# Kernel tuning notes

Measured on AMD Instinct MI355X. Metric: run time of the kernel, lower is better.

Reference implementation:

```python
import jax, jax.numpy as jnp
import numpy as np

MIN_SIZE = 25.0      # remove_small_boxes threshold (init default)
IOU_THRESH = 0.3     # nms iou_threshold (init default)
MAX_DET = 100        # rcnn_detections_per_image (init default)
IMG = 1024.0         # synthetic image size for box generation


def setup_inputs() -> dict:
    key = jax.random.key(0)
    k1, k2, k3 = jax.random.split(key, 3)
    B, N = 16, 4096
    # valid xyxy boxes inside a 1024x1024 image
    cxcy = jax.random.uniform(k1, (B, N, 2), minval=0.0, maxval=IMG)
    wh = jax.random.uniform(k2, (B, N, 2), minval=1.0, maxval=300.0)
    boxes = jnp.concatenate([cxcy - wh / 2, cxcy + wh / 2], axis=-1)
    boxes = jnp.clip(boxes, 0.0, IMG)
    scores = jax.random.uniform(k3, (B, N))
    return {"boxes": boxes, "scores": scores}


def _pairwise_iou(b):
    # b: [N,4] xyxy -> iou: [N,N]
    area = (b[:, 2] - b[:, 0]) * (b[:, 3] - b[:, 1])
    lt = jnp.maximum(b[:, None, :2], b[None, :, :2])
    rb = jnp.minimum(b[:, None, 2:], b[None, :, 2:])
    wh = jnp.clip(rb - lt, 0.0)
    inter = wh[..., 0] * wh[..., 1]
    return inter / (area[:, None] + area[None, :] - inter + 1e-9)


def _per_image(boxes, scores):
    # boxes [N,4], scores [N] -> (out_boxes [K,4], valid [K])
    N = boxes.shape[0]
    # remove_small_boxes: width and height >= min_size
    valid = ((boxes[:, 2] - boxes[:, 0]) >= MIN_SIZE) & ((boxes[:, 3] - boxes[:, 1]) >= MIN_SIZE)
    s = jnp.where(valid, scores, -jnp.inf)
    order = jnp.argsort(-s)          # score-descending, invalid boxes last
    b = boxes[order]
    v = valid[order]
    iou = _pairwise_iou(b)           # [N,N] dominant intermediate
    idx = jnp.arange(N)

    def body(i, keep):
        # greedy NMS: box i (if kept) suppresses lower-scored overlapping boxes
        sup = (iou[i] > IOU_THRESH) & keep[i] & (idx > i)
        return keep & ~sup

    keep = jax.lax.fori_loop(0, N, body, v)
    # first MAX_DET kept boxes in score order (fixed-shape top-k truncation)
    sel = jnp.argsort(jnp.where(keep, idx, N))[:MAX_DET]
    valid_out = jnp.take(keep, sel)
    out_boxes = jnp.where(valid_out[:, None], b[sel], 0.0)
    return out_boxes, valid_out


def reference(boxes, scores):
    # boxes [B,N,4], scores [B,N] -> [B,K,5] rows (image_idx, x1,y1,x2,y2);
    # padded rows have image_idx = -1 (fixed-shape analogue of the ragged concat)
    out_boxes, valid = jax.vmap(_per_image)(boxes, scores)
    B = boxes.shape[0]
    img_idx = jnp.where(valid, jnp.arange(B, dtype=boxes.dtype)[:, None], -1.0)
    return jnp.concatenate([img_idx[..., None], out_boxes], axis=-1)
```

## Files before the change

### kernel.cpp

```cpp
#include <hip/hip_runtime.h>
#include <math.h>

#define N_BOX 4096
#define B_IMG 16
#define MAXDET 100
#define MINSZ 25.0f
#define IOUT 0.3f
#define IG 16
#define JG 8
#define JW (N_BOX / JG)

__device__ __forceinline__ float iou_f(float ax1, float ay1, float ax2, float ay2, float aarea,
                                       float bx1, float by1, float bx2, float by2, float barea) {
#pragma clang fp contract(off)
    float lx = fmaxf(ax1, bx1);
    float ly = fmaxf(ay1, by1);
    float rx = fminf(ax2, bx2);
    float ry = fminf(ay2, by2);
    float wx = fmaxf(rx - lx, 0.0f);
    float wy = fmaxf(ry - ly, 0.0f);
    float inter = wx * wy;
    float denom = ((aarea + barea) - inter) + 1e-9f;
    return inter / denom;
}

__global__ __launch_bounds__(256) void key_kernel(
        const float4* __restrict__ boxes, const float* __restrict__ scores,
        unsigned long long* __restrict__ ckey) {
    int idx = blockIdx.x * 256 + threadIdx.x;
    float4 bx = boxes[idx];
    bool valid = ((bx.z - bx.x) >= MINSZ) && ((bx.w - bx.y) >= MINSZ);
    float k = valid ? scores[idx] : -INFINITY;
    unsigned u = __float_as_uint(k);
    u = (u & 0x80000000u) ? ~u : (u | 0x80000000u);
    int i = idx & (N_BOX - 1);
    ckey[idx] = ((unsigned long long)u << 12) | (unsigned long long)(N_BOX - 1 - i);
}

__global__ __launch_bounds__(256) void partial_rank_kernel(
        const unsigned long long* __restrict__ ckey, unsigned short* __restrict__ part) {
    int blk = blockIdx.x;
    int jg = blk & (JG - 1);
    int ig = (blk >> 3) & (IG - 1);
    int b  = blk >> 7;
    int t = threadIdx.x;
    int i = ig * 256 + t;
    unsigned long long ci = ckey[b * N_BOX + i];
    const unsigned long long* cj = ckey + b * N_BOX + jg * JW;
    int r = 0;
#pragma unroll 8
    for (int j = 0; j < JW; ++j)
        r += (cj[j] > ci) ? 1 : 0;
    part[(b * JG + jg) * N_BOX + i] = (unsigned short)r;
}

__global__ __launch_bounds__(256) void nms_kernel(
        const float4* __restrict__ boxes, const unsigned long long* __restrict__ ckey,
        const unsigned short* __restrict__ part, float* __restrict__ out) {
    __shared__ unsigned short sinv[N_BOX];
    __shared__ __align__(16) float4 kbox[384];
    __shared__ int scnt[4];
    int b = blockIdx.x;
    int t = threadIdx.x;
    int w = t >> 6, l = t & 63;
    const float4* bb = boxes + (size_t)b * N_BOX;

#pragma unroll
    for (int p = 0; p < 16; ++p) {
        int i = t + 256 * p;
        int rank = 0;
#pragma unroll
        for (int jg = 0; jg < JG; ++jg)
            rank += part[(b * JG + jg) * N_BOX + i];
        unsigned valid = (unsigned)(ckey[b * N_BOX + i] >> 43) & 1u;
        sinv[rank] = (unsigned short)(i | (valid << 15));
    }
    __syncthreads();

    int kept = 0;
    for (int g = 0; g < 16; ++g) {
        int c = g * 4 + w;
        unsigned short e = sinv[c * 64 + l];
        float4 bx = bb[e & 0xFFFu];
        float x1 = bx.x, y1 = bx.y, x2 = bx.z, y2 = bx.w;
        float ar;
        {
#pragma clang fp contract(off)
            ar = (x2 - x1) * (y2 - y1);
        }
        bool alive = (e >> 15) != 0;
        int K0 = kept;
        for (int q = 0; q < K0; ++q) {
            float4 kb = kbox[q];
            float kar;
            {
#pragma clang fp contract(off)
                kar = (kb.z - kb.x) * (kb.w - kb.y);
            }
            float v = iou_f(kb.x, kb.y, kb.z, kb.w, kar, x1, y1, x2, y2, ar);
            if (v > IOUT) alive = false;
        }
        for (int s = 0; s < 4; ++s) {
            if (w == s) {
                int Kcur = K0;
                for (int ss = 0; ss < s; ++ss) Kcur += scnt[ss];
                int cnt = 0;
                if (Kcur < MAXDET) {
                    for (int q = K0; q < Kcur; ++q) {
                        float4 kb = kbox[q];
                        float kar;
                        {
#pragma clang fp contract(off)
                            kar = (kb.z - kb.x) * (kb.w - kb.y);
                        }
                        float v = iou_f(kb.x, kb.y, kb.z, kb.w, kar, x1, y1, x2, y2, ar);
                        if (v > IOUT) alive = false;
                    }
                    unsigned long long m = __ballot(alive);
                    unsigned long long mm = m;
                    while (mm) {
                        int i = __ffsll(mm) - 1;
                        float bx1 = __shfl(x1, i), by1 = __shfl(y1, i);
                        float bx2 = __shfl(x2, i), by2 = __shfl(y2, i);
                        float ba  = __shfl(ar, i);
                        float v = iou_f(bx1, by1, bx2, by2, ba, x1, y1, x2, y2, ar);
                        bool sup = (l > i) && (v > IOUT) && ((m >> l) & 1ull);
                        unsigned long long sm = __ballot(sup);
                        m &= ~sm;
                        mm &= ~(1ull << i);
                        mm &= m;
                    }
                    cnt = __popcll(m);
                    int pos = Kcur + __popcll(m & ((1ull << l) - 1ull));
                    if ((m >> l) & 1ull) kbox[pos] = make_float4(x1, y1, x2, y2);
                }
                if (l == 0) scnt[s] = cnt;
            }
            __syncthreads();
        }
        kept = K0 + scnt[0] + scnt[1] + scnt[2] + scnt[3];
        __syncthreads();
        if (kept >= MAXDET) break;
    }

    int tot = kept < MAXDET ? kept : MAXDET;
    float* ob = out + (size_t)b * MAXDET * 5;
    for (int r = t; r < MAXDET; r += 256) {
        float* row = ob + r * 5;
        if (r < tot) {
            float4 kb = kbox[r];
            row[0] = (float)b;
            row[1] = kb.x; row[2] = kb.y; row[3] = kb.z; row[4] = kb.w;
        } else {
            row[0] = -1.0f;
            row[1] = 0.0f; row[2] = 0.0f; row[3] = 0.0f; row[4] = 0.0f;
        }
    }
}

extern "C" void kernel_launch(void* const* d_in, const int* in_sizes, int n_in,
                              void* d_out, int out_size, void* d_ws, size_t ws_size,
                              hipStream_t stream) {
    const float4* boxes = (const float4*)d_in[0];
    const float* scores = (const float*)d_in[1];
    float* out = (float*)d_out;

    unsigned long long* ckey = (unsigned long long*)d_ws;
    unsigned short* part     = (unsigned short*)((char*)d_ws + (size_t)524288);

    key_kernel<<<B_IMG * N_BOX / 256, 256, 0, stream>>>(boxes, scores, ckey);
    partial_rank_kernel<<<B_IMG * IG * JG, 256, 0, stream>>>(ckey, part);
    nms_kernel<<<B_IMG, 256, 0, stream>>>(boxes, ckey, part, out);
}
```

Before: 114.1 us.

## Fuse key, rank and NMS into one kernel using in-LDS bucket sort

Replaces the three-kernel pipeline (key, O(N^2) pairwise rank, NMS) with one per-image kernel. It builds sort keys in registers, bucket-sorts valid boxes by score into LDS via histogram, prefix scan and atomic scatter, then ranks each box only within its bucket. Invalid boxes are placed after all valid ones by ballot prefix counts. This removes the quadratic rank pass, the global workspace traffic and two launches. In exchange the sort runs on only 16 blocks, and the bucketing assumes scores lie in [0,1).

```diff
diff --git a/kernel.cpp b/kernel.cpp
--- a/kernel.cpp
+++ b/kernel.cpp
@@ -6,9 +6,7 @@
 #define MAXDET 100
 #define MINSZ 25.0f
 #define IOUT 0.3f
-#define IG 16
-#define JG 8
-#define JW (N_BOX / JG)
+#define NBUCK 1024
 
 __device__ __forceinline__ float iou_f(float ax1, float ay1, float ax2, float ay2, float aarea,
                                        float bx1, float by1, float bx2, float by2, float barea) {
@@ -24,56 +22,124 @@
     return inter / denom;
 }
 
-__global__ __launch_bounds__(256) void key_kernel(
+__global__ __launch_bounds__(256) void fused_kernel(
         const float4* __restrict__ boxes, const float* __restrict__ scores,
-        unsigned long long* __restrict__ ckey) {
-    int idx = blockIdx.x * 256 + threadIdx.x;
-    float4 bx = boxes[idx];
-    bool valid = ((bx.z - bx.x) >= MINSZ) && ((bx.w - bx.y) >= MINSZ);
-    float k = valid ? scores[idx] : -INFINITY;
-    unsigned u = __float_as_uint(k);
-    u = (u & 0x80000000u) ? ~u : (u | 0x80000000u);
-    int i = idx & (N_BOX - 1);
-    ckey[idx] = ((unsigned long long)u << 12) | (unsigned long long)(N_BOX - 1 - i);
-}
-
-__global__ __launch_bounds__(256) void partial_rank_kernel(
-        const unsigned long long* __restrict__ ckey, unsigned short* __restrict__ part) {
-    int blk = blockIdx.x;
-    int jg = blk & (JG - 1);
-    int ig = (blk >> 3) & (IG - 1);
-    int b  = blk >> 7;
-    int t = threadIdx.x;
-    int i = ig * 256 + t;
-    unsigned long long ci = ckey[b * N_BOX + i];
-    const unsigned long long* cj = ckey + b * N_BOX + jg * JW;
-    int r = 0;
-#pragma unroll 8
-    for (int j = 0; j < JW; ++j)
-        r += (cj[j] > ci) ? 1 : 0;
-    part[(b * JG + jg) * N_BOX + i] = (unsigned short)r;
-}
-
-__global__ __launch_bounds__(256) void nms_kernel(
-        const float4* __restrict__ boxes, const unsigned long long* __restrict__ ckey,
-        const unsigned short* __restrict__ part, float* __restrict__ out) {
+        float* __restrict__ out) {
+    __shared__ __align__(16) unsigned long long bkey[N_BOX];
     __shared__ unsigned short sinv[N_BOX];
+    __shared__ int cnt[NBUCK];
+    __shared__ int start[NBUCK];
+    __shared__ int chunkInv[64];
+    __shared__ int chunkPre[64];
+    __shared__ int scratch[256];
+    __shared__ int wsum[4];
+    __shared__ int nvalidS;
     __shared__ __align__(16) float4 kbox[384];
     __shared__ int scnt[4];
+
     int b = blockIdx.x;
     int t = threadIdx.x;
     int w = t >> 6, l = t & 63;
     const float4* bb = boxes + (size_t)b * N_BOX;
-
+    const float* ss = scores + (size_t)b * N_BOX;
+
+    for (int q = t; q < NBUCK; q += 256) cnt[q] = 0;
+    __syncthreads();
+
+    unsigned long long key[16];
+    int buck[16];
+    unsigned char ipre[16];
+    unsigned vmask = 0;
 #pragma unroll
     for (int p = 0; p < 16; ++p) {
-        int i = t + 256 * p;
-        int rank = 0;
-#pragma unroll
-        for (int jg = 0; jg < JG; ++jg)
-            rank += part[(b * JG + jg) * N_BOX + i];
-        unsigned valid = (unsigned)(ckey[b * N_BOX + i] >> 43) & 1u;
-        sinv[rank] = (unsigned short)(i | (valid << 15));
+        int i = w * 64 + 256 * p + l;
+        float4 bx = bb[i];
+        float sc = ss[i];
+        bool valid = ((bx.z - bx.x) >= MINSZ) && ((bx.w - bx.y) >= MINSZ);
+        float k = valid ? sc : -INFINITY;
+        unsigned u = __float_as_uint(k);
+        u = (u & 0x80000000u) ? ~u : (u | 0x80000000u);
+        key[p] = ((unsigned long long)u << 12) | (unsigned long long)(N_BOX - 1 - i);
+        unsigned long long im = __ballot(!valid);
+        ipre[p] = (unsigned char)__popcll(im & ((1ull << l) - 1ull));
+        if (l == 0) chunkInv[w + 4 * p] = __popcll(im);
+        if (valid) {
+            vmask |= (1u << p);
+            int bk = (int)(sc * 1024.0f);
+            bk = bk < 0 ? 0 : (bk > NBUCK - 1 ? NBUCK - 1 : bk);
+            buck[p] = bk;
+            atomicAdd(&cnt[bk], 1);
+        }
+    }
+    __syncthreads();
+
+    if (t < 64) {
+        int v = chunkInv[t];
+        int x = v;
+        for (int off = 1; off < 64; off <<= 1) {
+            int y = __shfl_up(x, off);
+            if (l >= off) x += y;
+        }
+        chunkPre[t] = x - v;
+        if (t == 63) nvalidS = N_BOX - x;
+    }
+    __syncthreads();
+
+    int S = 0;
+#pragma unroll
+    for (int q = 0; q < 4; ++q) S += cnt[t * 4 + q];
+    scratch[255 - t] = S;
+    __syncthreads();
+    int xv = scratch[t];
+    int incl = xv;
+    for (int off = 1; off < 64; off <<= 1) {
+        int y = __shfl_up(incl, off);
+        if (l >= off) incl += y;
+    }
+    if (l == 63) wsum[w] = incl;
+    __syncthreads();
+    int woff = 0;
+    for (int q = 0; q < w; ++q) woff += wsum[q];
+    int excl = woff + incl - xv;
+    __syncthreads();
+    scratch[t] = excl;
+    __syncthreads();
+    int T = scratch[255 - t];
+    int running = T;
+#pragma unroll
+    for (int q = 3; q >= 0; --q) {
+        start[t * 4 + q] = running;
+        running += cnt[t * 4 + q];
+    }
+    __syncthreads();
+
+#pragma unroll
+    for (int p = 0; p < 16; ++p) {
+        if (vmask & (1u << p)) {
+            int ps = atomicAdd(&start[buck[p]], 1);
+            bkey[ps] = key[p];
+        }
+    }
+    __syncthreads();
+
+    int nvalid = nvalidS;
+#pragma unroll
+    for (int p = 0; p < 16; ++p) {
+        int i = w * 64 + 256 * p + l;
+        int r;
+        unsigned vbit = (vmask >> p) & 1u;
+        if (vbit) {
+            int bk = buck[p];
+            int end = start[bk];
+            int beg = end - cnt[bk];
+            unsigned long long mk = key[p];
+            r = beg;
+            for (int q = beg; q < end; ++q)
+                r += (bkey[q] > mk) ? 1 : 0;
+        } else {
+            r = nvalid + chunkPre[w + 4 * p] + (int)ipre[p];
+        }
+        sinv[r] = (unsigned short)(i | (vbit << 15));
     }
     __syncthreads();
 
@@ -103,8 +169,8 @@
         for (int s = 0; s < 4; ++s) {
             if (w == s) {
                 int Kcur = K0;
-                for (int ss = 0; ss < s; ++ss) Kcur += scnt[ss];
-                int cnt = 0;
+                for (int ss2 = 0; ss2 < s; ++ss2) Kcur += scnt[ss2];
+                int cnt2 = 0;
                 if (Kcur < MAXDET) {
                     for (int q = K0; q < Kcur; ++q) {
                         float4 kb = kbox[q];
@@ -130,11 +196,11 @@
                         mm &= ~(1ull << i);
                         mm &= m;
                     }
-                    cnt = __popcll(m);
+                    cnt2 = __popcll(m);
                     int pos = Kcur + __popcll(m & ((1ull << l) - 1ull));
                     if ((m >> l) & 1ull) kbox[pos] = make_float4(x1, y1, x2, y2);
                 }
-                if (l == 0) scnt[s] = cnt;
+                if (l == 0) scnt[s] = cnt2;
             }
             __syncthreads();
         }
@@ -164,11 +230,7 @@
     const float4* boxes = (const float4*)d_in[0];
     const float* scores = (const float*)d_in[1];
     float* out = (float*)d_out;
-
-    unsigned long long* ckey = (unsigned long long*)d_ws;
-    unsigned short* part     = (unsigned short*)((char*)d_ws + (size_t)524288);
-
-    key_kernel<<<B_IMG * N_BOX / 256, 256, 0, stream>>>(boxes, scores, ckey);
-    partial_rank_kernel<<<B_IMG * IG * JG, 256, 0, stream>>>(ckey, part);
-    nms_kernel<<<B_IMG, 256, 0, stream>>>(boxes, ckey, part, out);
+    (void)d_ws; (void)ws_size;
+
+    fused_kernel<<<B_IMG, 256, 0, stream>>>(boxes, scores, out);
 }
```

Result: faster. 103.1 us (-9.6%).
